# Optimization experiments

Hardware: AMD Instinct MI355X
Metric: run time of the kernel (lower is better)

The kernel has to match this reference:

```python
import jax, jax.numpy as jnp
import numpy as np

H, W = 256, 832
B = 2
SEARCH_W, SEARCH_H = 7, 3
SPARSITY_RAD = 2
SENSE_RANGE = 10
PIX_W = 20.0          # pixel_distance_weight
ALPHA_W = 0.7         # alpha_distance_weight
MULLINE_W = 15.0      # pixel_mulline_distance_weight
ALPHA_PAD = 0.6       # alpha_padding
INF = 1e9


def _sorted_offsets(span_x, span_y):
    xs, ys = np.meshgrid(span_x, span_y)
    xs = xs.flatten(); ys = ys.flatten()
    order = np.argsort(xs ** 2 + ys ** 2, kind='stable')
    return xs[order].astype(np.int32), ys[order].astype(np.int32)


def setup_inputs() -> dict:
    key = jax.random.key(0)
    k1, k2 = jax.random.split(key)
    src = (jax.random.uniform(k1, (B, 1, H, W)) < 0.02).astype(jnp.float32)
    dst = (jax.random.uniform(k2, (B, 1, H, W)) < 0.02).astype(jnp.float32)
    xx, yy = _sorted_offsets(np.arange(-SEARCH_W, SEARCH_W + 1), np.arange(-SEARCH_H, SEARCH_H + 1))
    sxs, sys_ = np.meshgrid(np.arange(-SPARSITY_RAD, SPARSITY_RAD + 1), np.arange(-SPARSITY_RAD, SPARSITY_RAD + 1))
    sxx = sxs.flatten().astype(np.int32); syy = sys_.flatten().astype(np.int32)
    cxx, cyy = _sorted_offsets(np.arange(-SENSE_RANGE, SENSE_RANGE + 1), np.arange(-SENSE_RANGE, SENSE_RANGE + 1))
    return {"binMapsrc": src, "binMapdst": dst,
            "xx": jnp.asarray(xx), "yy": jnp.asarray(yy),
            "sxx": jnp.asarray(sxx), "syy": jnp.asarray(syy),
            "cxx": jnp.asarray(cxx), "cyy": jnp.asarray(cyy)}


def _orientation(m):
    # local edge orientation from a 3x3 box-blurred map
    b = sum(jnp.roll(jnp.roll(m, di, 0), dj, 1) for di in (-1, 0, 1) for dj in (-1, 0, 1))
    gy, gx = jnp.gradient(b)
    return jnp.arctan2(gy, gx)


def _morph_single(src, dst, xx, yy, sxx, syy, cxx, cyy):
    gy, gx = jnp.meshgrid(jnp.arange(H, dtype=jnp.int32), jnp.arange(W, dtype=jnp.int32), indexing='ij')

    def gather(offy, offx, arr, fill):
        ii = gy[None] + offy[:, None, None]          # [K,H,W]
        jj = gx[None] + offx[:, None, None]
        inb = (ii >= 0) & (ii < H) & (jj >= 0) & (jj < W)
        vals = arr[jnp.clip(ii, 0, H - 1), jnp.clip(jj, 0, W - 1)]
        return jnp.where(inb, vals, fill)

    src_e = src > 0.5
    # --- sparsify source edge points: keep min-linear-index edge in each sparsity window ---
    lin = jnp.where(src_e, (gy * W + gx).astype(jnp.float32), INF)
    keep = src_e & (lin == gather(syy, sxx, lin, INF).min(0))
    # --- windowed correspondence search with distance + orientation scoring ---
    theta_s = _orientation(src)
    theta_d = _orientation(dst)
    hit = gather(yy, xx, dst, 0.0) > 0.5             # [K,H,W]
    ang = 1.0 - jnp.cos(theta_s[None] - gather(yy, xx, theta_d, 0.0))
    dist = jnp.sqrt((xx * xx + yy * yy).astype(jnp.float32))
    score = jnp.where(hit, PIX_W * dist[:, None, None] + MULLINE_W * ALPHA_W * ang, INF)
    kbest = jnp.argmin(score, axis=0)                # [H,W]
    active = keep & (score.min(0) < 0.5 * INF)
    dispx = jnp.where(active, xx[kbest].astype(jnp.float32), 0.0)
    dispy = jnp.where(active, yy[kbest].astype(jnp.float32), 0.0)
    # --- diffuse sparse displacements over the sense window (scan keeps memory small) ---
    R = SENSE_RANGE
    pad = lambda a: jnp.pad(a, ((R, R), (R, R)))
    pdx, pdy, pm = pad(dispx), pad(dispy), pad(active.astype(jnp.float32))
    wk = jnp.exp(-jnp.sqrt((cxx * cxx + cyy * cyy).astype(jnp.float32)) / (0.5 * R))

    def body(carry, inp):
        nx, ny, den = carry
        dy_, dx_, w = inp
        sl = lambda a: jax.lax.dynamic_slice(a, (R + dy_, R + dx_), (H, W))
        return (nx + w * sl(pdx), ny + w * sl(pdy), den + w * sl(pm)), None

    zeros = jnp.zeros((H, W), jnp.float32)
    (nx, ny, den), _ = jax.lax.scan(body, (zeros, zeros, zeros), (cyy, cxx, wk))
    mdx = ALPHA_PAD * nx / (den + 1e-6)
    mdy = ALPHA_PAD * ny / (den + 1e-6)
    morphedx = gx.astype(jnp.float32) + mdx
    morphedy = gy.astype(jnp.float32) + mdy
    return jnp.stack([morphedx, morphedy], 0)        # [2,H,W]


def reference(binMapsrc, binMapdst, xx, yy, sxx, syy, cxx, cyy):
    f = lambda s, d: _morph_single(s, d, xx, yy, sxx, syy, cxx, cyy)
    return jax.vmap(f)(binMapsrc[:, 0], binMapdst[:, 0])  # [B,2,H,W]
```

## Files before the change

### kernel.cpp

```cpp
#include <hip/hip_runtime.h>
#include <math.h>

#define BB 2
#define HH 256
#define WW 832
#define HWIMG (HH * WW)

#define TS 16
#define TXN (WW / TS)
#define TYN (HH / TS)

#define KCAP 160
#define HCAP 192

#define SRH 40
#define SRW 64
#define DRH 46
#define DRW 64

__device__ inline float theta_at(const float* __restrict__ m, int i, int j) {
    int ri[5], cj[5];
#pragma unroll
    for (int t = 0; t < 5; ++t) {
        int r = i + t - 2; r = (r < 0) ? r + HH : (r >= HH ? r - HH : r);
        int c = j + t - 2; c = (c < 0) ? c + WW : (c >= WW ? c - WW : c);
        ri[t] = r * WW; cj[t] = c;
    }
    float S[5][5];
#pragma unroll
    for (int a = 0; a < 5; ++a)
#pragma unroll
        for (int c = 0; c < 5; ++c)
            S[a][c] = m[ri[a] + cj[c]];
    float ct[5], cm[5], cb[5];
#pragma unroll
    for (int c = 0; c < 5; ++c) {
        ct[c] = S[0][c] + S[1][c] + S[2][c];
        cm[c] = S[1][c] + S[2][c] + S[3][c];
        cb[c] = S[2][c] + S[3][c] + S[4][c];
    }
    float Bm = ct[1] + ct[2] + ct[3];
    float Bp = cb[1] + cb[2] + cb[3];
    float Bl = cm[0] + cm[1] + cm[2];
    float Br = cm[2] + cm[3] + cm[4];
    float Bc = cm[1] + cm[2] + cm[3];
    float gy = (i == 0) ? (Bp - Bc) : (i == HH - 1) ? (Bc - Bm) : 0.5f * (Bp - Bm);
    float gx = (j == 0) ? (Br - Bc) : (j == WW - 1) ? (Bc - Bl) : 0.5f * (Br - Bl);
    return atan2f(gy, gx);
}

__device__ inline float theta_lds(const float* __restrict__ m, int stride,
                                  int li, int lj) {
    const float* p = m + (li - 2) * stride + (lj - 2);
    float S[5][5];
#pragma unroll
    for (int a = 0; a < 5; ++a)
#pragma unroll
        for (int c = 0; c < 5; ++c)
            S[a][c] = p[a * stride + c];
    float ct[5], cm[5], cb[5];
#pragma unroll
    for (int c = 0; c < 5; ++c) {
        ct[c] = S[0][c] + S[1][c] + S[2][c];
        cm[c] = S[1][c] + S[2][c] + S[3][c];
        cb[c] = S[2][c] + S[3][c] + S[4][c];
    }
    float Bm = ct[1] + ct[2] + ct[3];
    float Bp = cb[1] + cb[2] + cb[3];
    float Bl = cm[0] + cm[1] + cm[2];
    float Br = cm[2] + cm[3] + cm[4];
    float gy = 0.5f * (Bp - Bm);
    float gx = 0.5f * (Br - Bl);
    return atan2f(gy, gx);
}

__global__ __launch_bounds__(256) void fused_kernel(
        const float* __restrict__ src, const float* __restrict__ dst,
        const int* __restrict__ xx, const int* __restrict__ yy, int K,
        float* __restrict__ out) {
    __shared__ float slds[SRH * SRW];
    __shared__ float dlds[DRH * DRW];
    __shared__ int kox[112], koy[112];
    __shared__ float kd[112];
    __shared__ float wt[441];
    __shared__ int recs[KCAP];
    __shared__ float tss[KCAP];
    __shared__ unsigned long long best64[KCAP];
    __shared__ int hits[HCAP];
    __shared__ int nkeep, nhit;

    int tid = threadIdx.x;
    int lane = tid & 63;
    int wv = tid >> 6;
    int b = blockIdx.z;
    int i0 = blockIdx.y * TS;
    int j0 = blockIdx.x * TS;
    const float* sb = src + b * HWIMG;
    const float* db = dst + b * HWIMG;

    if (tid == 0) { nkeep = 0; nhit = 0; }
    for (int t = tid; t < KCAP; t += 256) best64[t] = ~0ULL;

    float sv[10], dv[12];
    {
        int c = j0 - 12 + lane;
        int cc = min(max(c, 0), WW - 1);
        bool cok = (c >= 0) && (c < WW) && (lane < 40);
#pragma unroll
        for (int rr = 0; rr < 10; ++rr) {
            int r = i0 - 12 + wv + 4 * rr;
            int cr = min(max(r, 0), HH - 1);
            float v = cok ? sb[cr * WW + cc] : 0.f;
            sv[rr] = (r >= 0 && r < HH) ? v : 0.f;
        }
    }
    {
        int c = j0 - 20 + lane;
        int cc = min(max(c, 0), WW - 1);
        bool cok = (c >= 0) && (c < WW) && (lane < 55);
#pragma unroll
        for (int rr = 0; rr < 12; ++rr) {
            int row = wv + 4 * rr;
            int r = i0 - 15 + row;
            int cr = min(max(r, 0), HH - 1);
            float v = (cok && row < DRH) ? db[cr * WW + cc] : 0.f;
            dv[rr] = (r >= 0 && r < HH) ? v : 0.f;
        }
    }
#pragma unroll
    for (int rr = 0; rr < 10; ++rr)
        slds[(wv + 4 * rr) * SRW + lane] = sv[rr];
#pragma unroll
    for (int rr = 0; rr < 12; ++rr)
        if (wv + 4 * rr < DRH) dlds[(wv + 4 * rr) * DRW + lane] = dv[rr];

    if (tid < K) {
        int ox = xx[tid], oy = yy[tid];
        kox[tid] = ox; koy[tid] = oy;
        kd[tid] = 20.0f * sqrtf((float)(ox * ox + oy * oy));
    }
    for (int t = tid; t < 21 * 32; t += 256) {
        int dy = t >> 5, dx = t & 31;
        if (dx < 21)
            wt[dy * 21 + dx] = expf(-sqrtf((float)((dx - 10) * (dx - 10) +
                                                   (dy - 10) * (dy - 10))) / 5.0f);
    }
    __syncthreads();

    for (int t = tid; t < 36 * 64; t += 256) {
        int cl = t & 63, rl = t >> 6;
        if (cl < 36) {
            int li = rl + 2, lj = cl + 2;
            if (slds[li * SRW + lj] > 0.5f) {
                float m = 0.f;
#pragma unroll
                for (int p = 0; p < 12; ++p) {
                    int di = (p < 5) ? -2 : (p < 10 ? -1 : 0);
                    int dj = (p < 5) ? (p - 2) : (p < 10 ? (p - 7) : (p - 12));
                    m = fmaxf(m, slds[(li + di) * SRW + (lj + dj)]);
                }
                if (m <= 0.5f) {
                    int gi = i0 - 10 + rl, gj = j0 - 10 + cl;
                    int p = atomicAdd(&nkeep, 1);
                    if (p < KCAP) recs[p] = gj | (gi << 10);
                }
            }
        }
    }
    __syncthreads();

    int nk = (nkeep < KCAP) ? nkeep : KCAP;
    for (int t = tid; t < nk; t += 256) {
        int rec = recs[t];
        int kj = rec & 1023, ki = rec >> 10;
        bool inner = (ki >= 2) && (ki < HH - 2) && (kj >= 2) && (kj < WW - 2);
        tss[t] = inner ? theta_lds(slds, SRW, ki - i0 + 12, kj - j0 + 12)
                       : theta_at(sb, ki, kj);
    }
    for (int t = tid; t < nk * 128; t += 256) {
        int w = t >> 7, k = t & 127;
        if (k < K) {
            int rec = recs[w];
            int pli = (rec >> 10) - i0 + 15 + koy[k];
            int plj = (rec & 1023) - j0 + 20 + kox[k];
            if (dlds[pli * DRW + plj] > 0.5f) {
                int p = atomicAdd(&nhit, 1);
                if (p < HCAP) hits[p] = (w << 7) | k;
            }
        }
    }
    __syncthreads();

    int nh = (nhit < HCAP) ? nhit : HCAP;
    for (int t = tid; t < nh; t += 256) {
        int w = hits[t] >> 7, k = hits[t] & 127;
        int rec = recs[w];
        int pi = (rec >> 10) + koy[k], pj = (rec & 1023) + kox[k];
        bool inner = (pi >= 2) && (pi < HH - 2) && (pj >= 2) && (pj < WW - 2);
        float td = inner ? theta_lds(dlds, DRW, pi - i0 + 15, pj - j0 + 20)
                         : theta_at(db, pi, pj);
        float sc = kd[k] + 10.5f * (1.0f - cosf(tss[w] - td));
        unsigned long long pk =
            ((unsigned long long)__float_as_uint(sc) << 32) | (unsigned)k;
        atomicMin(&best64[w], pk);
    }
    __syncthreads();

    int gj = j0 + (tid & 15);
    int gi = i0 + (tid >> 4);
    float nx = 0.f, ny = 0.f, de = 0.f;
    for (int w = 0; w < nk; ++w) {
        unsigned long long v = best64[w];
        if (v != ~0ULL) {
            int rec = recs[w];
            int dj = (rec & 1023) - gj;
            int di = (rec >> 10) - gi;
            if (dj >= -10 && dj <= 10 && di >= -10 && di <= 10) {
                int k = (int)(v & 127ULL);
                float w_ = wt[(di + 10) * 21 + dj + 10];
                de += w_; nx += w_ * (float)kox[k]; ny += w_ * (float)koy[k];
            }
        }
    }
    float inv = 0.6f / (de + 1e-6f);
    int obase = b * 2 * HWIMG;
    out[obase + gi * WW + gj] = (float)gj + nx * inv;
    out[obase + HWIMG + gi * WW + gj] = (float)gi + ny * inv;
}

extern "C" void kernel_launch(void* const* d_in, const int* in_sizes, int n_in,
                              void* d_out, int out_size, void* d_ws, size_t ws_size,
                              hipStream_t stream) {
    const float* src = (const float*)d_in[0];
    const float* dst = (const float*)d_in[1];
    const int* xx = (const int*)d_in[2];
    const int* yy = (const int*)d_in[3];
    int K = in_sizes[2];

    float* out = (float*)d_out;
    dim3 grid(TXN, TYN, BB);
    fused_kernel<<<grid, dim3(256), 0, stream>>>(src, dst, xx, yy, K, out);
}
```

Measured before the change: 92.18 us.

## Store edge maps as bytes in LDS and remap tiles across XCDs

Source and destination halo windows are stored in shared memory as 8-bit binary masks instead of floats. Each thread loads four floats and packs them into one 32-bit word, and sparsity scanning skips 4-pixel groups that hold no edges. The 3D grid becomes a 1D grid with a tile remap that groups neighbouring tiles onto the same XCD chunk, aiming at better L2 reuse of overlapping halos. This shrinks LDS use and the number of LDS reads, at the cost of thresholding during the load and more index arithmetic.

After: 89.44 us (median of 2 runs). 1.03x faster.

```diff
diff --git a/kernel.cpp b/kernel.cpp
--- a/kernel.cpp
+++ b/kernel.cpp
@@ -7,8 +7,10 @@
 #define HWIMG (HH * WW)
 
 #define TS 16
-#define TXN (WW / TS)
-#define TYN (HH / TS)
+#define TXN 52
+#define TYN 16
+#define NTILE (TXN * TYN * BB)
+#define CHUNK (NTILE / 8)
 
 #define KCAP 160
 #define HCAP 192
@@ -49,15 +51,15 @@
     return atan2f(gy, gx);
 }
 
-__device__ inline float theta_lds(const float* __restrict__ m, int stride,
-                                  int li, int lj) {
-    const float* p = m + (li - 2) * stride + (lj - 2);
+__device__ inline float theta_lds_u8(const unsigned char* __restrict__ m,
+                                     int stride, int li, int lj) {
+    const unsigned char* p = m + (li - 2) * stride + (lj - 2);
     float S[5][5];
 #pragma unroll
     for (int a = 0; a < 5; ++a)
 #pragma unroll
         for (int c = 0; c < 5; ++c)
-            S[a][c] = p[a * stride + c];
+            S[a][c] = (float)p[a * stride + c];
     float ct[5], cm[5], cb[5];
 #pragma unroll
     for (int c = 0; c < 5; ++c) {
@@ -78,8 +80,8 @@
         const float* __restrict__ src, const float* __restrict__ dst,
         const int* __restrict__ xx, const int* __restrict__ yy, int K,
         float* __restrict__ out) {
-    __shared__ float slds[SRH * SRW];
-    __shared__ float dlds[DRH * DRW];
+    __shared__ unsigned char slds8[SRH * SRW];
+    __shared__ unsigned char dlds8[DRH * DRW];
     __shared__ int kox[112], koy[112];
     __shared__ float kd[112];
     __shared__ float wt[441];
@@ -90,50 +92,67 @@
     __shared__ int nkeep, nhit;
 
     int tid = threadIdx.x;
-    int lane = tid & 63;
-    int wv = tid >> 6;
-    int b = blockIdx.z;
-    int i0 = blockIdx.y * TS;
-    int j0 = blockIdx.x * TS;
+    int lin = blockIdx.x;
+    int tile = (lin & 7) * CHUNK + (lin >> 3);
+    int bz = tile / (TXN * TYN);
+    int rem = tile - bz * (TXN * TYN);
+    int by = rem / TXN;
+    int bx = rem - by * TXN;
+    int b = bz;
+    int i0 = by * TS;
+    int j0 = bx * TS;
     const float* sb = src + b * HWIMG;
     const float* db = dst + b * HWIMG;
 
     if (tid == 0) { nkeep = 0; nhit = 0; }
     for (int t = tid; t < KCAP; t += 256) best64[t] = ~0ULL;
 
-    float sv[10], dv[12];
-    {
-        int c = j0 - 12 + lane;
-        int cc = min(max(c, 0), WW - 1);
-        bool cok = (c >= 0) && (c < WW) && (lane < 40);
-#pragma unroll
-        for (int rr = 0; rr < 10; ++rr) {
-            int r = i0 - 12 + wv + 4 * rr;
-            int cr = min(max(r, 0), HH - 1);
-            float v = cok ? sb[cr * WW + cc] : 0.f;
-            sv[rr] = (r >= 0 && r < HH) ? v : 0.f;
-        }
-    }
-    {
-        int c = j0 - 20 + lane;
-        int cc = min(max(c, 0), WW - 1);
-        bool cok = (c >= 0) && (c < WW) && (lane < 55);
-#pragma unroll
-        for (int rr = 0; rr < 12; ++rr) {
-            int row = wv + 4 * rr;
-            int r = i0 - 15 + row;
-            int cr = min(max(r, 0), HH - 1);
-            float v = (cok && row < DRH) ? db[cr * WW + cc] : 0.f;
-            dv[rr] = (r >= 0 && r < HH) ? v : 0.f;
-        }
-    }
-#pragma unroll
-    for (int rr = 0; rr < 10; ++rr)
-        slds[(wv + 4 * rr) * SRW + lane] = sv[rr];
-#pragma unroll
-    for (int rr = 0; rr < 12; ++rr)
-        if (wv + 4 * rr < DRH) dlds[(wv + 4 * rr) * DRW + lane] = dv[rr];
-
+#pragma unroll
+    for (int it = 0; it < 3; ++it) {
+        int t = tid + it * 256;
+        if (t < SRH * 16) {
+            int row = t >> 4, sl = t & 15;
+            if (sl < 11) {
+                int r = i0 - 12 + row;
+                int cr = min(max(r, 0), HH - 1);
+                bool rok = (r >= 0) && (r < HH);
+                const float* rp = sb + cr * WW;
+                unsigned pk = 0;
+#pragma unroll
+                for (int e = 0; e < 4; ++e) {
+                    int c = j0 - 14 + 4 * sl + e;
+                    int cc = min(max(c, 0), WW - 1);
+                    float v = rp[cc];
+                    unsigned bit = (rok && c >= 0 && c < WW && v > 0.5f) ? 1u : 0u;
+                    pk |= bit << (8 * e);
+                }
+                *(unsigned*)&slds8[row * SRW + 4 * sl] = pk;
+            }
+        }
+    }
+#pragma unroll
+    for (int it = 0; it < 3; ++it) {
+        int t = tid + it * 256;
+        if (t < DRH * 16) {
+            int row = t >> 4, sl = t & 15;
+            if (sl < 14) {
+                int r = i0 - 15 + row;
+                int cr = min(max(r, 0), HH - 1);
+                bool rok = (r >= 0) && (r < HH);
+                const float* rp = db + cr * WW;
+                unsigned pk = 0;
+#pragma unroll
+                for (int e = 0; e < 4; ++e) {
+                    int c = j0 - 20 + 4 * sl + e;
+                    int cc = min(max(c, 0), WW - 1);
+                    float v = rp[cc];
+                    unsigned bit = (rok && c >= 0 && c < WW && v > 0.5f) ? 1u : 0u;
+                    pk |= bit << (8 * e);
+                }
+                *(unsigned*)&dlds8[row * DRW + 4 * sl] = pk;
+            }
+        }
+    }
     if (tid < K) {
         int ox = xx[tid], oy = yy[tid];
         kox[tid] = ox; koy[tid] = oy;
@@ -147,22 +166,29 @@
     }
     __syncthreads();
 
-    for (int t = tid; t < 36 * 64; t += 256) {
-        int cl = t & 63, rl = t >> 6;
-        if (cl < 36) {
-            int li = rl + 2, lj = cl + 2;
-            if (slds[li * SRW + lj] > 0.5f) {
-                float m = 0.f;
-#pragma unroll
-                for (int p = 0; p < 12; ++p) {
-                    int di = (p < 5) ? -2 : (p < 10 ? -1 : 0);
-                    int dj = (p < 5) ? (p - 2) : (p < 10 ? (p - 7) : (p - 12));
-                    m = fmaxf(m, slds[(li + di) * SRW + (lj + dj)]);
-                }
-                if (m <= 0.5f) {
-                    int gi = i0 - 10 + rl, gj = j0 - 10 + cl;
-                    int p = atomicAdd(&nkeep, 1);
-                    if (p < KCAP) recs[p] = gj | (gi << 10);
+    for (int t = tid; t < 36 * 16; t += 256) {
+        int rl = t >> 4, c4 = t & 15;
+        if (c4 < 9) {
+            unsigned w32 = *(const unsigned*)&slds8[(rl + 2) * SRW + 4 + 4 * c4];
+            if (w32) {
+#pragma unroll
+                for (int e = 0; e < 4; ++e) {
+                    if ((w32 >> (8 * e)) & 1) {
+                        int cl = 4 * c4 + e;
+                        int li = rl + 2, lj = cl + 4;
+                        unsigned m = 0;
+#pragma unroll
+                        for (int p = 0; p < 12; ++p) {
+                            int di = (p < 5) ? -2 : (p < 10 ? -1 : 0);
+                            int dj = (p < 5) ? (p - 2) : (p < 10 ? (p - 7) : (p - 12));
+                            m |= slds8[(li + di) * SRW + (lj + dj)];
+                        }
+                        if (!m) {
+                            int gi = i0 - 10 + rl, gj = j0 - 10 + cl;
+                            int p = atomicAdd(&nkeep, 1);
+                            if (p < KCAP) recs[p] = gj | (gi << 10);
+                        }
+                    }
                 }
             }
         }
@@ -174,7 +200,7 @@
         int rec = recs[t];
         int kj = rec & 1023, ki = rec >> 10;
         bool inner = (ki >= 2) && (ki < HH - 2) && (kj >= 2) && (kj < WW - 2);
-        tss[t] = inner ? theta_lds(slds, SRW, ki - i0 + 12, kj - j0 + 12)
+        tss[t] = inner ? theta_lds_u8(slds8, SRW, ki - i0 + 12, kj - j0 + 14)
                        : theta_at(sb, ki, kj);
     }
     for (int t = tid; t < nk * 128; t += 256) {
@@ -183,7 +209,7 @@
             int rec = recs[w];
             int pli = (rec >> 10) - i0 + 15 + koy[k];
             int plj = (rec & 1023) - j0 + 20 + kox[k];
-            if (dlds[pli * DRW + plj] > 0.5f) {
+            if (dlds8[pli * DRW + plj]) {
                 int p = atomicAdd(&nhit, 1);
                 if (p < HCAP) hits[p] = (w << 7) | k;
             }
@@ -197,7 +223,7 @@
         int rec = recs[w];
         int pi = (rec >> 10) + koy[k], pj = (rec & 1023) + kox[k];
         bool inner = (pi >= 2) && (pi < HH - 2) && (pj >= 2) && (pj < WW - 2);
-        float td = inner ? theta_lds(dlds, DRW, pi - i0 + 15, pj - j0 + 20)
+        float td = inner ? theta_lds_u8(dlds8, DRW, pi - i0 + 15, pj - j0 + 20)
                          : theta_at(db, pi, pj);
         float sc = kd[k] + 10.5f * (1.0f - cosf(tss[w] - td));
         unsigned long long pk =
@@ -238,6 +264,5 @@
     int K = in_sizes[2];
 
     float* out = (float*)d_out;
-    dim3 grid(TXN, TYN, BB);
-    fused_kernel<<<grid, dim3(256), 0, stream>>>(src, dst, xx, yy, K, out);
-}
+    fused_kernel<<<dim3(NTILE), dim3(256), 0, stream>>>(src, dst, xx, yy, K, out);
+}
```

## Pack edge maps into LDS bitmasks and search matches per keypoint via bit scans

Applied to the files above, without the earlier changes.

The float LDS tiles for the source and destination maps are replaced with 64-bit per-row ballot bitmasks. Sparsification now uses bitwise neighbourhood tests, and the match search walks the set bits in a 15x7 window per kept point. That removes the per-offset hit list, the atomicMin on packed scores and one barrier. The best offset is packed into a single 32-bit entry, and the launch becomes a 1D grid with tiles interleaved across chunks of eight. In exchange, one thread now serially scans all candidates for its keypoint, which can cause load imbalance, and the tie-break is emulated through a kof lookup table.

Result: no change. 92.12 us (-0.1%).

```diff
diff --git a/kernel.cpp b/kernel.cpp
--- a/kernel.cpp
+++ b/kernel.cpp
@@ -7,16 +7,15 @@
 #define HWIMG (HH * WW)
 
 #define TS 16
-#define TXN (WW / TS)
-#define TYN (HH / TS)
+#define TXN 52
+#define TYN 16
+#define NTILE (TXN * TYN * BB)
+#define CHUNK (NTILE / 8)
 
 #define KCAP 160
-#define HCAP 192
-
-#define SRH 40
-#define SRW 64
-#define DRH 46
-#define DRW 64
+
+#define SBR 40
+#define DBR 46
 
 __device__ inline float theta_at(const float* __restrict__ m, int i, int j) {
     int ri[5], cj[5];
@@ -49,15 +48,16 @@
     return atan2f(gy, gx);
 }
 
-__device__ inline float theta_lds(const float* __restrict__ m, int stride,
-                                  int li, int lj) {
-    const float* p = m + (li - 2) * stride + (lj - 2);
+__device__ inline float theta_bits(const unsigned long long* __restrict__ rows,
+                                   int r0, int b0) {
     float S[5][5];
 #pragma unroll
-    for (int a = 0; a < 5; ++a)
+    for (int a = 0; a < 5; ++a) {
+        unsigned long long w = rows[r0 + a] >> b0;
 #pragma unroll
         for (int c = 0; c < 5; ++c)
-            S[a][c] = p[a * stride + c];
+            S[a][c] = (float)((unsigned)(w >> c) & 1u);
+    }
     float ct[5], cm[5], cb[5];
 #pragma unroll
     for (int c = 0; c < 5; ++c) {
@@ -78,67 +78,61 @@
         const float* __restrict__ src, const float* __restrict__ dst,
         const int* __restrict__ xx, const int* __restrict__ yy, int K,
         float* __restrict__ out) {
-    __shared__ float slds[SRH * SRW];
-    __shared__ float dlds[DRH * DRW];
-    __shared__ int kox[112], koy[112];
-    __shared__ float kd[112];
+    __shared__ unsigned long long sbits[SBR];
+    __shared__ unsigned long long dbits[DBR];
     __shared__ float wt[441];
+    __shared__ unsigned char kof[128];
     __shared__ int recs[KCAP];
-    __shared__ float tss[KCAP];
-    __shared__ unsigned long long best64[KCAP];
-    __shared__ int hits[HCAP];
-    __shared__ int nkeep, nhit;
+    __shared__ unsigned ents[KCAP];
+    __shared__ int nkeep;
 
     int tid = threadIdx.x;
     int lane = tid & 63;
     int wv = tid >> 6;
-    int b = blockIdx.z;
-    int i0 = blockIdx.y * TS;
-    int j0 = blockIdx.x * TS;
+    int lin = blockIdx.x;
+    int tile = (lin & 7) * CHUNK + (lin >> 3);
+    int b = tile / (TXN * TYN);
+    int rem = tile - b * (TXN * TYN);
+    int by = rem / TXN;
+    int bx = rem - by * TXN;
+    int i0 = by * TS;
+    int j0 = bx * TS;
     const float* sb = src + b * HWIMG;
     const float* db = dst + b * HWIMG;
 
-    if (tid == 0) { nkeep = 0; nhit = 0; }
-    for (int t = tid; t < KCAP; t += 256) best64[t] = ~0ULL;
-
-    float sv[10], dv[12];
+    if (tid == 0) nkeep = 0;
+
     {
-        int c = j0 - 12 + lane;
+        int c = j0 - 14 + lane;
         int cc = min(max(c, 0), WW - 1);
-        bool cok = (c >= 0) && (c < WW) && (lane < 40);
+        bool cok = (c >= 0) && (c < WW);
 #pragma unroll
         for (int rr = 0; rr < 10; ++rr) {
-            int r = i0 - 12 + wv + 4 * rr;
+            int row = wv + 4 * rr;
+            int r = i0 - 12 + row;
             int cr = min(max(r, 0), HH - 1);
-            float v = cok ? sb[cr * WW + cc] : 0.f;
-            sv[rr] = (r >= 0 && r < HH) ? v : 0.f;
+            float v = sb[cr * WW + cc];
+            unsigned long long m = __ballot(cok && r >= 0 && r < HH && v > 0.5f);
+            if (lane == 0) sbits[row] = m;
         }
     }
     {
         int c = j0 - 20 + lane;
         int cc = min(max(c, 0), WW - 1);
-        bool cok = (c >= 0) && (c < WW) && (lane < 55);
+        bool cok = (c >= 0) && (c < WW);
 #pragma unroll
         for (int rr = 0; rr < 12; ++rr) {
             int row = wv + 4 * rr;
             int r = i0 - 15 + row;
             int cr = min(max(r, 0), HH - 1);
-            float v = (cok && row < DRH) ? db[cr * WW + cc] : 0.f;
-            dv[rr] = (r >= 0 && r < HH) ? v : 0.f;
-        }
-    }
-#pragma unroll
-    for (int rr = 0; rr < 10; ++rr)
-        slds[(wv + 4 * rr) * SRW + lane] = sv[rr];
-#pragma unroll
-    for (int rr = 0; rr < 12; ++rr)
-        if (wv + 4 * rr < DRH) dlds[(wv + 4 * rr) * DRW + lane] = dv[rr];
-
-    if (tid < K) {
-        int ox = xx[tid], oy = yy[tid];
-        kox[tid] = ox; koy[tid] = oy;
-        kd[tid] = 20.0f * sqrtf((float)(ox * ox + oy * oy));
-    }
+            float v = db[cr * WW + cc];
+            unsigned long long m =
+                __ballot(row < DBR && cok && r >= 0 && r < HH && v > 0.5f);
+            if (lane == 0 && row < DBR) dbits[row] = m;
+        }
+    }
+    if (tid < K)
+        kof[(yy[tid] + 3) * 15 + (xx[tid] + 7)] = (unsigned char)tid;
     for (int t = tid; t < 21 * 32; t += 256) {
         int dy = t >> 5, dx = t & 31;
         if (dx < 21)
@@ -147,23 +141,20 @@
     }
     __syncthreads();
 
-    for (int t = tid; t < 36 * 64; t += 256) {
-        int cl = t & 63, rl = t >> 6;
-        if (cl < 36) {
-            int li = rl + 2, lj = cl + 2;
-            if (slds[li * SRW + lj] > 0.5f) {
-                float m = 0.f;
-#pragma unroll
-                for (int p = 0; p < 12; ++p) {
-                    int di = (p < 5) ? -2 : (p < 10 ? -1 : 0);
-                    int dj = (p < 5) ? (p - 2) : (p < 10 ? (p - 7) : (p - 12));
-                    m = fmaxf(m, slds[(li + di) * SRW + (lj + dj)]);
-                }
-                if (m <= 0.5f) {
-                    int gi = i0 - 10 + rl, gj = j0 - 10 + cl;
-                    int p = atomicAdd(&nkeep, 1);
-                    if (p < KCAP) recs[p] = gj | (gi << 10);
-                }
+    if (tid < 36) {
+        unsigned long long rm2 = sbits[tid];
+        unsigned long long rm1 = sbits[tid + 1];
+        unsigned long long rc = sbits[tid + 2];
+        unsigned long long em = rc & 0x000000FFFFFFFFF0ULL;
+        while (em) {
+            int bpos = __builtin_ctzll(em);
+            em &= em - 1;
+            unsigned nb = (unsigned)((((rm2 | rm1) >> (bpos - 2)) & 0x1FULL)
+                                     | ((rc >> (bpos - 2)) & 0x3ULL));
+            if (!nb) {
+                int gi = i0 - 10 + tid, gj = j0 - 14 + bpos;
+                int p = atomicAdd(&nkeep, 1);
+                if (p < KCAP) recs[p] = gj | (gi << 10);
             }
         }
     }
@@ -173,36 +164,35 @@
     for (int t = tid; t < nk; t += 256) {
         int rec = recs[t];
         int kj = rec & 1023, ki = rec >> 10;
-        bool inner = (ki >= 2) && (ki < HH - 2) && (kj >= 2) && (kj < WW - 2);
-        tss[t] = inner ? theta_lds(slds, SRW, ki - i0 + 12, kj - j0 + 12)
-                       : theta_at(sb, ki, kj);
-    }
-    for (int t = tid; t < nk * 128; t += 256) {
-        int w = t >> 7, k = t & 127;
-        if (k < K) {
-            int rec = recs[w];
-            int pli = (rec >> 10) - i0 + 15 + koy[k];
-            int plj = (rec & 1023) - j0 + 20 + kox[k];
-            if (dlds[pli * DRW + plj] > 0.5f) {
-                int p = atomicAdd(&nhit, 1);
-                if (p < HCAP) hits[p] = (w << 7) | k;
+        bool innerS = (ki >= 2) && (ki < HH - 2) && (kj >= 2) && (kj < WW - 2);
+        float ts = innerS ? theta_bits(sbits, ki - i0 + 10, kj - j0 + 12)
+                          : theta_at(sb, ki, kj);
+        int klj = kj - j0 + 20;
+        float best = 1e9f;
+        int bk = 1 << 20, bdx = 0, bdy = 0;
+        for (int dy = -3; dy <= 3; ++dy) {
+            unsigned win = (unsigned)((dbits[ki + dy - i0 + 15] >> (klj - 7))
+                                      & 0x7FFFULL);
+            while (win) {
+                int e = __builtin_ctz(win);
+                win &= win - 1;
+                int dx = e - 7;
+                int pi = ki + dy, pj = kj + dx;
+                bool innerD = (pi >= 2) && (pi < HH - 2) &&
+                              (pj >= 2) && (pj < WW - 2);
+                float td = innerD ? theta_bits(dbits, pi - i0 + 13, pj - j0 + 18)
+                                  : theta_at(db, pi, pj);
+                float sc = 20.0f * sqrtf((float)(dx * dx + dy * dy))
+                         + 10.5f * (1.0f - cosf(ts - td));
+                int k = kof[(dy + 3) * 15 + (dx + 7)];
+                if (sc < best || (sc == best && k < bk)) {
+                    best = sc; bk = k; bdx = dx; bdy = dy;
+                }
             }
         }
-    }
-    __syncthreads();
-
-    int nh = (nhit < HCAP) ? nhit : HCAP;
-    for (int t = tid; t < nh; t += 256) {
-        int w = hits[t] >> 7, k = hits[t] & 127;
-        int rec = recs[w];
-        int pi = (rec >> 10) + koy[k], pj = (rec & 1023) + kox[k];
-        bool inner = (pi >= 2) && (pi < HH - 2) && (pj >= 2) && (pj < WW - 2);
-        float td = inner ? theta_lds(dlds, DRW, pi - i0 + 15, pj - j0 + 20)
-                         : theta_at(db, pi, pj);
-        float sc = kd[k] + 10.5f * (1.0f - cosf(tss[w] - td));
-        unsigned long long pk =
-            ((unsigned long long)__float_as_uint(sc) << 32) | (unsigned)k;
-        atomicMin(&best64[w], pk);
+        ents[t] = (best < 5e8f)
+            ? (unsigned)(rec | ((bdx + 7) << 18) | ((bdy + 3) << 22))
+            : 0xFFFFFFFFu;
     }
     __syncthreads();
 
@@ -210,15 +200,15 @@
     int gi = i0 + (tid >> 4);
     float nx = 0.f, ny = 0.f, de = 0.f;
     for (int w = 0; w < nk; ++w) {
-        unsigned long long v = best64[w];
-        if (v != ~0ULL) {
-            int rec = recs[w];
-            int dj = (rec & 1023) - gj;
-            int di = (rec >> 10) - gi;
+        unsigned p = ents[w];
+        if (p != 0xFFFFFFFFu) {
+            int dj = (int)(p & 1023) - gj;
+            int di = (int)((p >> 10) & 255) - gi;
             if (dj >= -10 && dj <= 10 && di >= -10 && di <= 10) {
-                int k = (int)(v & 127ULL);
                 float w_ = wt[(di + 10) * 21 + dj + 10];
-                de += w_; nx += w_ * (float)kox[k]; ny += w_ * (float)koy[k];
+                de += w_;
+                nx += w_ * (float)((int)((p >> 18) & 15) - 7);
+                ny += w_ * (float)((int)((p >> 22) & 7) - 3);
             }
         }
     }
@@ -238,6 +228,5 @@
     int K = in_sizes[2];
 
     float* out = (float*)d_out;
-    dim3 grid(TXN, TYN, BB);
-    fused_kernel<<<grid, dim3(256), 0, stream>>>(src, dst, xx, yy, K, out);
-}
+    fused_kernel<<<dim3(NTILE), dim3(256), 0, stream>>>(src, dst, xx, yy, K, out);
+}
```
